# Kernel optimization log

Measured on AMD Instinct MI355X. Metric: run time of the kernel, lower is better.

## Reference

```python
import jax, jax.numpy as jnp
import numpy as np

B, LQ, LKV = 32, 512, 512
SIZE, H = 512, 8
HD = SIZE // H
SCALE = 1.0 / np.sqrt(HD)
LN_EPS = 1e-5


def layer_norm(x, w, b):
    mu = jnp.mean(x, axis=-1, keepdims=True)
    var = jnp.mean(jnp.square(x - mu), axis=-1, keepdims=True)
    return (x - mu) * jax.lax.rsqrt(var + LN_EPS) * w + b


def setup_inputs() -> dict:
    key = jax.random.key(0)
    ks = jax.random.split(key, 8)
    s = 0.02
    return {
        "query": jax.random.normal(ks[0], (B, LQ, SIZE), jnp.float32),
        "key_value": jax.random.normal(ks[1], (B, LKV, SIZE), jnp.float32),
        "Wq": jax.random.normal(ks[2], (SIZE, SIZE), jnp.float32) * s,
        "bq": jnp.zeros((SIZE,), jnp.float32),
        "Wk": jax.random.normal(ks[3], (SIZE, SIZE), jnp.float32) * s,
        "bk": jnp.zeros((SIZE,), jnp.float32),
        "Wv": jax.random.normal(ks[4], (SIZE, SIZE), jnp.float32) * s,
        "bv": jnp.zeros((SIZE,), jnp.float32),
        "Wo": jax.random.normal(ks[5], (SIZE, SIZE), jnp.float32) * s,
        "bo": jnp.zeros((SIZE,), jnp.float32),
        "ln0_w": jnp.ones((SIZE,), jnp.float32),
        "ln0_b": jnp.zeros((SIZE,), jnp.float32),
        "ln1_w": jnp.ones((SIZE,), jnp.float32),
        "ln1_b": jnp.zeros((SIZE,), jnp.float32),
    }


def reference(query, key_value, Wq, bq, Wk, bk, Wv, bv, Wo, bo, ln0_w, ln0_b, ln1_w, ln1_b):
    b, lq, _ = query.shape
    lkv = key_value.shape[1]
    # projections
    q = query @ Wq.T + bq          # [B, Lq, SIZE]
    k = key_value @ Wk.T + bk      # [B, Lkv, SIZE]
    v = key_value @ Wv.T + bv
    # split heads: torch cat(split(head_size, 2), 0) == [B,L,H,HD] view with head axis separate
    qh = q.reshape(b, lq, H, HD)
    kh = k.reshape(b, lkv, H, HD)
    vh = v.reshape(b, lkv, H, HD)
    # attention scores [B, H, Lq, Lkv]
    A_ = jnp.einsum("bqhd,bkhd->bhqk", qh, kh) * SCALE
    # signed softmax: tanh(A_) * softmax(sqrt(A_^2 + 0.01)) over keys
    A = jnp.tanh(A_) * jax.nn.softmax(jnp.sqrt(jnp.square(A_) + 0.01), axis=-1)
    # residual q + attention output, merge heads back
    oh = qh + jnp.einsum("bhqk,bkhd->bqhd", A, vh)   # [B, Lq, H, HD]
    output = oh.reshape(b, lq, SIZE)
    output = layer_norm(output, ln0_w, ln0_b)
    output = output + jax.nn.relu(output @ Wo.T + bo)
    output = layer_norm(output, ln1_w, ln1_b)
    return output
```

## Files before the change

kernel.cpp:

```cpp
#include <hip/hip_runtime.h>

#define SIZE_D 512
#define HEADS  8
#define HDIM   64
#define BATCH  32
#define SEQ    512
#define SCALE_F 0.125f
#define NROWS  (BATCH * SEQ)

typedef __attribute__((ext_vector_type(8))) short bf16x8;
typedef __attribute__((ext_vector_type(4))) float f32x4;
typedef __attribute__((ext_vector_type(4))) unsigned int u32x4;

__device__ __forceinline__ unsigned short f2bf(float f) {
    union { float f; unsigned int u; } c{f};
    unsigned int x = c.u;
    x += 0x7fffu + ((x >> 16) & 1u);
    return (unsigned short)(x >> 16);
}
__device__ __forceinline__ float bf2f(unsigned short u) {
    union { unsigned int i; float f; } c;
    c.i = (unsigned int)u << 16;
    return c.f;
}
__device__ __forceinline__ unsigned int pack2bf(float lo, float hi) {
    return ((__float_as_uint(hi) + 0x8000u) & 0xffff0000u) |
           ((__float_as_uint(lo) + 0x8000u) >> 16);
}
__device__ __forceinline__ void gload_lds16(const unsigned short* g, unsigned short* l) {
    __builtin_amdgcn_global_load_lds(
        (const __attribute__((address_space(1))) unsigned int*)g,
        (__attribute__((address_space(3))) unsigned int*)l, 16, 0, 0);
}

#define KBAR8() do {                                                      \
    asm volatile("s_waitcnt vmcnt(8) lgkmcnt(0)" ::: "memory");           \
    __builtin_amdgcn_sched_barrier(0);                                    \
    __builtin_amdgcn_s_barrier();                                         \
    __builtin_amdgcn_sched_barrier(0);                                    \
} while (0)
#define KBAR0() do {                                                      \
    asm volatile("s_waitcnt vmcnt(0) lgkmcnt(0)" ::: "memory");           \
    __builtin_amdgcn_sched_barrier(0);                                    \
    __builtin_amdgcn_s_barrier();                                         \
    __builtin_amdgcn_sched_barrier(0);                                    \
} while (0)

__global__ __launch_bounds__(256) void cvt_w4(const float* __restrict__ w0,
                                              const float* __restrict__ w1,
                                              const float* __restrict__ w2,
                                              const float* __restrict__ w3,
                                              unsigned short* __restrict__ d) {
    const float* srcs[4] = {w0, w1, w2, w3};
    const float* s = srcs[blockIdx.y];
    unsigned short* dst = d + (size_t)blockIdx.y * (SIZE_D * SIZE_D);
    const int n = SIZE_D * SIZE_D;
    const int stride = gridDim.x * blockDim.x * 4;
    for (int i = (blockIdx.x * blockDim.x + threadIdx.x) * 4; i < n; i += stride) {
        const float4 v = *reinterpret_cast<const float4*>(s + i);
        ushort4 o;
        o.x = f2bf(v.x); o.y = f2bf(v.y); o.z = f2bf(v.z); o.w = f2bf(v.w);
        *reinterpret_cast<ushort4*>(dst + i) = o;
    }
}

__global__ __launch_bounds__(256, 2) void gemm_proj3(const float* __restrict__ query,
                                                     const float* __restrict__ keyv,
                                                     const unsigned short* __restrict__ Wall,
                                                     const float* __restrict__ bq,
                                                     const float* __restrict__ bk,
                                                     const float* __restrict__ bv,
                                                     unsigned short* __restrict__ Qh,
                                                     unsigned short* __restrict__ Kh,
                                                     unsigned short* __restrict__ Vt) {
    __shared__ __align__(16) unsigned short Ad[2][128 * 64];
    __shared__ __align__(16) unsigned short Bd[2][128 * 64];

    const int tid  = threadIdx.x;
    const int wv   = tid >> 6;
    const int lane = tid & 63;
    const int y    = blockIdx.y;
    const int bm   = blockIdx.x * 128;
    const int bn   = y * 128;
    const int wr   = wv >> 1;
    const int wc   = wv & 1;

    const float* A = (y < 4) ? query : keyv;

    float4 areg[2][4][2];

    auto loadA = [&](int t, int slot) {
        const int k0 = t * 64;
#pragma unroll
        for (int i = 0; i < 4; ++i) {
            const int o   = (wv * 32 + i * 8) * 128 + lane * 16;
            const int row = o >> 7;
            const int col = ((o & 127) ^ ((row & 7) << 4)) >> 1;
            const float* src = A + (size_t)(bm + row) * SIZE_D + k0 + col;
            areg[slot][i][0] = *reinterpret_cast<const float4*>(src);
            areg[slot][i][1] = *reinterpret_cast<const float4*>(src + 4);
        }
    };
    auto writeA = [&](int buf, int slot) {
#pragma unroll
        for (int i = 0; i < 4; ++i) {
            const int o = (wv * 32 + i * 8) * 128 + lane * 16;
            union { unsigned int u[4]; bf16x8 v; } pk;
            pk.u[0] = pack2bf(areg[slot][i][0].x, areg[slot][i][0].y);
            pk.u[1] = pack2bf(areg[slot][i][0].z, areg[slot][i][0].w);
            pk.u[2] = pack2bf(areg[slot][i][1].x, areg[slot][i][1].y);
            pk.u[3] = pack2bf(areg[slot][i][1].z, areg[slot][i][1].w);
            *reinterpret_cast<bf16x8*>(&Ad[buf][o >> 1]) = pk.v;
        }
    };
    auto stageW = [&](int buf, int t) {
        const int k0 = t * 64;
#pragma unroll
        for (int i = 0; i < 4; ++i) {
            const int o   = (wv * 32 + i * 8) * 128 + lane * 16;
            const int row = o >> 7;
            const int col = ((o & 127) ^ ((row & 7) << 4)) >> 1;
            gload_lds16(Wall + (size_t)(bn + row) * SIZE_D + k0 + col, &Bd[buf][o >> 1]);
        }
    };

    f32x4 acc[4][4];
#pragma unroll
    for (int mt = 0; mt < 4; ++mt)
#pragma unroll
        for (int nt = 0; nt < 4; ++nt) acc[mt][nt] = (f32x4){0.f, 0.f, 0.f, 0.f};

    loadA(0, 0);
    stageW(0, 0);
    writeA(0, 0);
    loadA(1, 1);

#pragma unroll
    for (int t = 0; t < 8; ++t) {
        const int cur = t & 1;
        if (t < 7) { KBAR8(); } else { KBAR0(); }

        if (t < 7) stageW(cur ^ 1, t + 1);
        if (t < 6) loadA(t + 2, t & 1);

        bf16x8 af[2][4], bfr[2][4];
#pragma unroll
        for (int kc = 0; kc < 2; ++kc) {
#pragma unroll
            for (int mt = 0; mt < 4; ++mt) {
                const int r = wr * 64 + mt * 16 + (lane & 15);
                int byte = r * 128 + kc * 64 + (lane >> 4) * 16;
                byte ^= (r & 7) << 4;
                af[kc][mt] = *reinterpret_cast<const bf16x8*>(
                    reinterpret_cast<const char*>(&Ad[cur][0]) + byte);
            }
#pragma unroll
            for (int nt = 0; nt < 4; ++nt) {
                const int r = wc * 64 + nt * 16 + (lane & 15);
                int byte = r * 128 + kc * 64 + (lane >> 4) * 16;
                byte ^= (r & 7) << 4;
                bfr[kc][nt] = *reinterpret_cast<const bf16x8*>(
                    reinterpret_cast<const char*>(&Bd[cur][0]) + byte);
            }
        }
#pragma unroll
        for (int kc = 0; kc < 2; ++kc)
#pragma unroll
            for (int mt = 0; mt < 4; ++mt)
#pragma unroll
                for (int nt = 0; nt < 4; ++nt)
                    acc[mt][nt] = __builtin_amdgcn_mfma_f32_16x16x32_bf16(
                        af[kc][mt], bfr[kc][nt], acc[mt][nt], 0, 0, 0);

        if (t < 7) writeA(cur ^ 1, (t + 1) & 1);
    }

    if (y < 8) {
        const float* bias = (y < 4) ? bq : bk;
        unsigned short* D = (y < 4) ? Qh : Kh;
        const int coff = (y < 4) ? 0 : 512;
#pragma unroll
        for (int nt = 0; nt < 4; ++nt) {
            const int colL = bn - coff + wc * 64 + nt * 16 + (lane & 15);
            const float bc = bias[colL];
            const int h = colL >> 6, dd = colL & 63;
#pragma unroll
            for (int mt = 0; mt < 4; ++mt) {
                const int row0 = bm + wr * 64 + mt * 16 + (lane >> 4) * 4;
#pragma unroll
                for (int r = 0; r < 4; ++r) {
                    const int row = row0 + r;
                    const int b_ = row >> 9, l = row & 511;
                    float z = acc[mt][nt][r] + bc;
                    if (y >= 4) z *= SCALE_F;
                    D[(((size_t)b_ * HEADS + h) * SEQ + l) * HDIM + dd] = f2bf(z);
                }
            }
        }
    } else {
#pragma unroll
        for (int nt = 0; nt < 4; ++nt) {
            const int c2 = bn - 1024 + wc * 64 + nt * 16 + (lane & 15);
            const float bc = bv[c2];
            const int hV = c2 >> 6, dV = c2 & 63;
#pragma unroll
            for (int mt = 0; mt < 4; ++mt) {
                const int row0 = bm + wr * 64 + mt * 16 + (lane >> 4) * 4;
                const int b_ = row0 >> 9, kv = row0 & 511;
                ushort4 pk;
                pk.x = f2bf(acc[mt][nt][0] + bc);
                pk.y = f2bf(acc[mt][nt][1] + bc);
                pk.z = f2bf(acc[mt][nt][2] + bc);
                pk.w = f2bf(acc[mt][nt][3] + bc);
                *reinterpret_cast<ushort4*>(
                    &Vt[(((size_t)b_ * HEADS + hV) * HDIM + dV) * SEQ + kv]) = pk;
            }
        }
    }
}

__global__ __launch_bounds__(256, 2) void attn_mfma(const unsigned short* __restrict__ Qh,
                                                    const unsigned short* __restrict__ Kh,
                                                    const unsigned short* __restrict__ Vt,
                                                    unsigned short* __restrict__ outb) {
    __shared__ __align__(16) unsigned short Kt[2][64 * 64];
    __shared__ __align__(16) unsigned short Vs[2][64 * 64];

    const int tid  = threadIdx.x;
    const int wv   = tid >> 6;
    const int lane = tid & 63;
    const int bh   = blockIdx.x;
    const int b    = bh >> 3;
    const int h    = bh & 7;
    const int g    = lane >> 4;

    const unsigned short* Qb = Qh + (size_t)bh * (SEQ * HDIM);
    const unsigned short* Kb = Kh + (size_t)bh * (SEQ * HDIM);
    const unsigned short* Vb = Vt + (size_t)bh * (HDIM * SEQ);

    const int m0 = blockIdx.y * 256 + wv * 64;

    auto stageKV = [&](int buf, int t) {
        const int kv0 = t * 64;
#pragma unroll
        for (int i = 0; i < 2; ++i) {
            const int o   = i * 4096 + tid * 16;
            const int row = o >> 7;
            const int in  = (o & 127) ^ ((row & 7) << 4);
            gload_lds16(Kb + (size_t)(kv0 + row) * HDIM + (in >> 1), &Kt[buf][o >> 1]);
            gload_lds16(Vb + (size_t)row * SEQ + kv0 + (in >> 1), &Vs[buf][o >> 1]);
        }
    };

    bf16x8 qf[4][2];
#pragma unroll
    for (int mt = 0; mt < 4; ++mt)
#pragma unroll
        for (int kc = 0; kc < 2; ++kc) {
            const int m = m0 + mt * 16 + (lane & 15);
            union { u32x4 u; bf16x8 v; } cv;
            cv.u = *reinterpret_cast<const u32x4*>(
                Qb + (size_t)m * HDIM + kc * 32 + g * 8);
            qf[mt][kc] = cv.v;
        }

    f32x4 oacc[4][4];
    float esum[4] = {0.f, 0.f, 0.f, 0.f};
#pragma unroll
    for (int mt = 0; mt < 4; ++mt)
#pragma unroll
        for (int x = 0; x < 4; ++x) oacc[mt][x] = (f32x4){0.f, 0.f, 0.f, 0.f};

    stageKV(0, 0);
    __syncthreads();
    int cur = 0;

    for (int t = 0; t < 8; ++t) {
        if (t < 7) stageKV(cur ^ 1, t + 1);

        f32x4 sacc[4][4];
#pragma unroll
        for (int nt = 0; nt < 4; ++nt)
#pragma unroll
            for (int mt = 0; mt < 4; ++mt) sacc[nt][mt] = (f32x4){0.f, 0.f, 0.f, 0.f};

#pragma unroll
        for (int kc = 0; kc < 2; ++kc) {
            bf16x8 kf[4];
#pragma unroll
            for (int nt = 0; nt < 4; ++nt) {
                const int kvl = nt * 16 + (lane & 15);
                int byte = kvl * 128 + kc * 64 + g * 16;
                byte ^= (kvl & 7) << 4;
                kf[nt] = *reinterpret_cast<const bf16x8*>(
                    reinterpret_cast<const char*>(&Kt[cur][0]) + byte);
            }
            __builtin_amdgcn_s_setprio(1);
#pragma unroll
            for (int nt = 0; nt < 4; ++nt)
#pragma unroll
                for (int mt = 0; mt < 4; ++mt)
                    sacc[nt][mt] = __builtin_amdgcn_mfma_f32_16x16x32_bf16(
                        kf[nt], qf[mt][kc], sacc[nt][mt], 0, 0, 0);
            __builtin_amdgcn_s_setprio(0);
        }

        bf16x8 pa[2][4];
#pragma unroll
        for (int c = 0; c < 2; ++c)
#pragma unroll
            for (int mt = 0; mt < 4; ++mt) {
                float w[8];
#pragma unroll
                for (int j = 0; j < 8; ++j) {
                    const float s  = sacc[2 * c + (j >> 2)][mt][j & 3];
                    const float a  = fminf(fabsf(s), 30.0f);
                    const float tt = __expf(a);
                    const float t2 = tt * tt;
                    const float u  = __builtin_amdgcn_sqrtf(fmaf(s, s, 0.01f));
                    const float dl = u - a;
                    const float ed = fmaf(dl, fmaf(dl, 0.5f, 1.0f), 1.0f);
                    const float eu = tt * ed;
                    esum[mt] += eu;
                    const float th = fmaf(-2.0f, __builtin_amdgcn_rcpf(t2 + 1.0f), 1.0f);
                    w[j] = __builtin_copysignf(th * eu, s);
                }
                union { unsigned int u[4]; bf16x8 v; } pk;
#pragma unroll
                for (int p = 0; p < 4; ++p)
                    pk.u[p] = (__float_as_uint(w[2 * p + 1]) & 0xffff0000u) |
                              (__float_as_uint(w[2 * p]) >> 16);
                pa[c][mt] = pk.v;
            }

#pragma unroll
        for (int c = 0; c < 2; ++c) {
            bf16x8 vf[4];
#pragma unroll
            for (int dt = 0; dt < 4; ++dt) {
                const int d = dt * 16 + (lane & 15);
                const int swz = (d & 7) << 4;
                const int rowb = d * 128;
                uint2 lo = *reinterpret_cast<const uint2*>(
                    reinterpret_cast<const char*>(&Vs[cur][0]) +
                    (rowb + (((c * 32 + 4 * g) * 2) ^ swz)));
                uint2 hi = *reinterpret_cast<const uint2*>(
                    reinterpret_cast<const char*>(&Vs[cur][0]) +
                    (rowb + (((c * 32 + 16 + 4 * g) * 2) ^ swz)));
                union { unsigned int u[4]; bf16x8 v; } cvb;
                cvb.u[0] = lo.x; cvb.u[1] = lo.y;
                cvb.u[2] = hi.x; cvb.u[3] = hi.y;
                vf[dt] = cvb.v;
            }
            __builtin_amdgcn_s_setprio(1);
#pragma unroll
            for (int mt = 0; mt < 4; ++mt)
#pragma unroll
                for (int dt = 0; dt < 4; ++dt)
                    oacc[mt][dt] = __builtin_amdgcn_mfma_f32_16x16x32_bf16(
                        pa[c][mt], vf[dt], oacc[mt][dt], 0, 0, 0);
            __builtin_amdgcn_s_setprio(0);
        }

        __syncthreads();
        cur ^= 1;
    }

    float rden[4];
#pragma unroll
    for (int mt = 0; mt < 4; ++mt) {
        float e = esum[mt];
        e += __shfl_xor(e, 16);
        e += __shfl_xor(e, 32);
        rden[mt] = __builtin_amdgcn_rcpf(e);
    }
    float rr_[4][4];
#pragma unroll
    for (int mt = 0; mt < 4; ++mt)
#pragma unroll
        for (int r = 0; r < 4; ++r)
            rr_[mt][r] = __shfl(rden[mt], g * 4 + r);

#pragma unroll
    for (int mt = 0; mt < 4; ++mt)
#pragma unroll
        for (int dt = 0; dt < 4; ++dt)
#pragma unroll
            for (int r = 0; r < 4; ++r) {
                const int m = m0 + mt * 16 + g * 4 + r;
                const int d = dt * 16 + (lane & 15);
                const float qv = bf2f(Qb[(size_t)m * HDIM + d]);
                outb[((size_t)b * SEQ + m) * SIZE_D + h * HDIM + d] =
                    f2bf(qv + oacc[mt][dt][r] * rr_[mt][r]);
            }
}

__global__ __launch_bounds__(256) void ln0_bf16(const unsigned short* __restrict__ in,
                                                const float* __restrict__ w,
                                                const float* __restrict__ b,
                                                unsigned short* __restrict__ outb) {
    const int row = blockIdx.x;
    const int tid = threadIdx.x;
    const ushort2 xb = *reinterpret_cast<const ushort2*>(&in[(size_t)row * SIZE_D + tid * 2]);
    float2 x;
    x.x = bf2f(xb.x);
    x.y = bf2f(xb.y);

    float s  = x.x + x.y;
    float sq = x.x * x.x + x.y * x.y;
#pragma unroll
    for (int off = 32; off > 0; off >>= 1) {
        s  += __shfl_xor(s, off);
        sq += __shfl_xor(sq, off);
    }
    __shared__ float rs[4], rq[4];
    const int wv = tid >> 6;
    if ((tid & 63) == 0) { rs[wv] = s; rq[wv] = sq; }
    __syncthreads();
    s  = rs[0] + rs[1] + rs[2] + rs[3];
    sq = rq[0] + rq[1] + rq[2] + rq[3];

    const float mu  = s * (1.0f / SIZE_D);
    const float var = sq * (1.0f / SIZE_D) - mu * mu;
    const float rr  = rsqrtf(var + 1e-5f);

    const float2 wv2 = *reinterpret_cast<const float2*>(&w[tid * 2]);
    const float2 bv2 = *reinterpret_cast<const float2*>(&b[tid * 2]);
    ushort2 ob;
    ob.x = f2bf((x.x - mu) * rr * wv2.x + bv2.x);
    ob.y = f2bf((x.y - mu) * rr * wv2.y + bv2.y);
    *reinterpret_cast<ushort2*>(&outb[(size_t)row * SIZE_D + tid * 2]) = ob;
}

__global__ __launch_bounds__(512, 2) void oproj_ln(const unsigned short* __restrict__ X,
                                                   const unsigned short* __restrict__ W,
                                                   const float* __restrict__ bo,
                                                   const float* __restrict__ g1,
                                                   const float* __restrict__ b1,
                                                   float* __restrict__ out) {
    __shared__ __align__(16) unsigned short Ad[2][32 * 32];
    __shared__ __align__(16) unsigned short Bd[2][512 * 32];
    __shared__ float red[32][8][2];
    __shared__ float stat[32][2];

    const int tid  = threadIdx.x;
    const int wv   = tid >> 6;
    const int lane = tid & 63;
    const int bm   = blockIdx.x * 32;

    auto stage = [&](int buf, int t) {
        const int k0 = t * 32;
        if (tid < 128) {
            const int o   = tid * 16;
            const int row = o >> 6;
            const int in  = (o & 63) ^ (((row >> 1) & 3) << 4);
            gload_lds16(X + (size_t)(bm + row) * SIZE_D + k0 + (in >> 1), &Ad[buf][o >> 1]);
        }
#pragma unroll
        for (int i = 0; i < 4; ++i) {
            const int o   = i * 8192 + tid * 16;
            const int row = o >> 6;
            const int in  = (o & 63) ^ (((row >> 1) & 3) << 4);
            gload_lds16(W + (size_t)row * SIZE_D + k0 + (in >> 1), &Bd[buf][o >> 1]);
        }
    };

    f32x4 acc[2][4];
#pragma unroll
    for (int mt = 0; mt < 2; ++mt)
#pragma unroll
        for (int nt = 0; nt < 4; ++nt) acc[mt][nt] = (f32x4){0.f, 0.f, 0.f, 0.f};

    stage(0, 0);
    __syncthreads();
    int cur = 0;

    for (int t = 0; t < 16; ++t) {
        if (t < 15) stage(cur ^ 1, t + 1);

        bf16x8 af[2], bfr[4];
#pragma unroll
        for (int mt = 0; mt < 2; ++mt) {
            const int r = mt * 16 + (lane & 15);
            int byte = r * 64 + (lane >> 4) * 16;
            byte ^= ((r >> 1) & 3) << 4;
            af[mt] = *reinterpret_cast<const bf16x8*>(
                reinterpret_cast<const char*>(&Ad[cur][0]) + byte);
        }
#pragma unroll
        for (int nt = 0; nt < 4; ++nt) {
            const int r = wv * 64 + nt * 16 + (lane & 15);
            int byte = r * 64 + (lane >> 4) * 16;
            byte ^= ((r >> 1) & 3) << 4;
            bfr[nt] = *reinterpret_cast<const bf16x8*>(
                reinterpret_cast<const char*>(&Bd[cur][0]) + byte);
        }
#pragma unroll
        for (int mt = 0; mt < 2; ++mt)
#pragma unroll
            for (int nt = 0; nt < 4; ++nt)
                acc[mt][nt] = __builtin_amdgcn_mfma_f32_16x16x32_bf16(
                    af[mt], bfr[nt], acc[mt][nt], 0, 0, 0);

        __syncthreads();
        cur ^= 1;
    }

#pragma unroll
    for (int nt = 0; nt < 4; ++nt) {
        const int n  = wv * 64 + nt * 16 + (lane & 15);
        const float bc = bo[n];
#pragma unroll
        for (int mt = 0; mt < 2; ++mt) {
            const int row0 = bm + mt * 16 + (lane >> 4) * 4;
#pragma unroll
            for (int r = 0; r < 4; ++r) {
                const float R = bf2f(X[(size_t)(row0 + r) * SIZE_D + n]);
                acc[mt][nt][r] = R + fmaxf(acc[mt][nt][r] + bc, 0.0f);
            }
        }
    }

    float ps[2][4], pq[2][4];
#pragma unroll
    for (int mt = 0; mt < 2; ++mt)
#pragma unroll
        for (int r = 0; r < 4; ++r) {
            float s = 0.f, q = 0.f;
#pragma unroll
            for (int nt = 0; nt < 4; ++nt) {
                const float v = acc[mt][nt][r];
                s += v; q += v * v;
            }
#pragma unroll
            for (int off = 1; off <= 8; off <<= 1) {
                s += __shfl_xor(s, off);
                q += __shfl_xor(q, off);
            }
            ps[mt][r] = s; pq[mt][r] = q;
        }
    if ((lane & 15) < 8) {
        const int mtw = (lane & 15) >> 2;
        const int rw  = lane & 3;
        const int rowL = mtw * 16 + (lane >> 4) * 4 + rw;
        red[rowL][wv][0] = ps[mtw][rw];
        red[rowL][wv][1] = pq[mtw][rw];
    }
    __syncthreads();
    if (tid < 32) {
        float s = 0.f, q = 0.f;
#pragma unroll
        for (int w8 = 0; w8 < 8; ++w8) { s += red[tid][w8][0]; q += red[tid][w8][1]; }
        const float mu  = s * (1.0f / SIZE_D);
        const float var = q * (1.0f / SIZE_D) - mu * mu;
        stat[tid][0] = mu;
        stat[tid][1] = rsqrtf(var + 1e-5f);
    }
    __syncthreads();

#pragma unroll
    for (int nt = 0; nt < 4; ++nt) {
        const int n = wv * 64 + nt * 16 + (lane & 15);
        const float g = g1[n], bb = b1[n];
#pragma unroll
        for (int mt = 0; mt < 2; ++mt) {
#pragma unroll
            for (int r = 0; r < 4; ++r) {
                const int rowL = mt * 16 + (lane >> 4) * 4 + r;
                const float y = (acc[mt][nt][r] - stat[rowL][0]) * stat[rowL][1];
                out[(size_t)(bm + rowL) * SIZE_D + n] = y * g + bb;
            }
        }
    }
}

extern "C" void kernel_launch(void* const* d_in, const int* in_sizes, int n_in,
                              void* d_out, int out_size, void* d_ws, size_t ws_size,
                              hipStream_t stream) {
    const float* query = (const float*)d_in[0];
    const float* keyv  = (const float*)d_in[1];
    const float* Wq    = (const float*)d_in[2];
    const float* bq    = (const float*)d_in[3];
    const float* Wk    = (const float*)d_in[4];
    const float* bk    = (const float*)d_in[5];
    const float* Wv    = (const float*)d_in[6];
    const float* bv    = (const float*)d_in[7];
    const float* Wo    = (const float*)d_in[8];
    const float* bo    = (const float*)d_in[9];
    const float* ln0w  = (const float*)d_in[10];
    const float* ln0b  = (const float*)d_in[11];
    const float* ln1w  = (const float*)d_in[12];
    const float* ln1b  = (const float*)d_in[13];
    float* out = (float*)d_out;

    char* ws = (char*)d_ws;
    unsigned short* obf  = (unsigned short*)ws;
    unsigned short* Qh   = (unsigned short*)(ws + ((size_t)32 << 20));
    unsigned short* Xbf  = Qh;
    unsigned short* Kh   = (unsigned short*)(ws + ((size_t)48 << 20));
    unsigned short* Vt   = (unsigned short*)(ws + ((size_t)64 << 20));
    unsigned short* Wbf  = (unsigned short*)(ws + ((size_t)80 << 20));
    unsigned short* WoB  = Wbf + 786432;

    cvt_w4<<<dim3(64, 4), 256, 0, stream>>>(Wq, Wk, Wv, Wo, Wbf);

    gemm_proj3<<<dim3(128, 12), 256, 0, stream>>>(query, keyv, Wbf, bq, bk, bv, Qh, Kh, Vt);

    attn_mfma<<<dim3(BATCH * HEADS, 2), 256, 0, stream>>>(Qh, Kh, Vt, obf);

    ln0_bf16<<<NROWS, 256, 0, stream>>>(obf, ln0w, ln0b, Xbf);

    oproj_ln<<<NROWS / 32, 512, 0, stream>>>(Xbf, WoB, bo, ln1w, ln1b, out);
}
```

Baseline: 154.8 us.

## Quad-buffer attention KV tiles, halve barriers, and use one wave per row in LN0

The attention kernel now keeps four KV tile buffers in shared memory and stages two tiles ahead, processing two tiles per barrier, so there are half as many __syncthreads and loads have more time to overlap with compute. The clamp on |s| before exp is removed, which saves an instruction but could overflow if scores grow large. LayerNorm0 now gives each row to a single wavefront with 8-element vector loads, which removes the shared-memory reduction and block barrier and launches a quarter as many blocks. Doubling LDS per block to 64KB may reduce attention occupancy.

```diff
diff --git a/kernel.cpp b/kernel.cpp
--- a/kernel.cpp
+++ b/kernel.cpp
@@ -223,8 +223,8 @@
                                                     const unsigned short* __restrict__ Kh,
                                                     const unsigned short* __restrict__ Vt,
                                                     unsigned short* __restrict__ outb) {
-    __shared__ __align__(16) unsigned short Kt[2][64 * 64];
-    __shared__ __align__(16) unsigned short Vs[2][64 * 64];
+    __shared__ __align__(16) unsigned short Kt[4][64 * 64];
+    __shared__ __align__(16) unsigned short Vs[4][64 * 64];
 
     const int tid  = threadIdx.x;
     const int wv   = tid >> 6;
@@ -272,98 +272,105 @@
         for (int x = 0; x < 4; ++x) oacc[mt][x] = (f32x4){0.f, 0.f, 0.f, 0.f};
 
     stageKV(0, 0);
+    stageKV(1, 1);
     __syncthreads();
-    int cur = 0;
-
-    for (int t = 0; t < 8; ++t) {
-        if (t < 7) stageKV(cur ^ 1, t + 1);
-
-        f32x4 sacc[4][4];
-#pragma unroll
-        for (int nt = 0; nt < 4; ++nt)
-#pragma unroll
-            for (int mt = 0; mt < 4; ++mt) sacc[nt][mt] = (f32x4){0.f, 0.f, 0.f, 0.f};
-
-#pragma unroll
-        for (int kc = 0; kc < 2; ++kc) {
-            bf16x8 kf[4];
-#pragma unroll
-            for (int nt = 0; nt < 4; ++nt) {
-                const int kvl = nt * 16 + (lane & 15);
-                int byte = kvl * 128 + kc * 64 + g * 16;
-                byte ^= (kvl & 7) << 4;
-                kf[nt] = *reinterpret_cast<const bf16x8*>(
-                    reinterpret_cast<const char*>(&Kt[cur][0]) + byte);
-            }
-            __builtin_amdgcn_s_setprio(1);
+
+    for (int tt = 0; tt < 8; tt += 2) {
+        if (tt < 6) {
+            stageKV((tt + 2) & 3, tt + 2);
+            stageKV((tt + 3) & 3, tt + 3);
+        }
+
+#pragma unroll
+        for (int p = 0; p < 2; ++p) {
+            const int cur = (tt + p) & 3;
+
+            f32x4 sacc[4][4];
 #pragma unroll
             for (int nt = 0; nt < 4; ++nt)
 #pragma unroll
+                for (int mt = 0; mt < 4; ++mt) sacc[nt][mt] = (f32x4){0.f, 0.f, 0.f, 0.f};
+
+#pragma unroll
+            for (int kc = 0; kc < 2; ++kc) {
+                bf16x8 kf[4];
+#pragma unroll
+                for (int nt = 0; nt < 4; ++nt) {
+                    const int kvl = nt * 16 + (lane & 15);
+                    int byte = kvl * 128 + kc * 64 + g * 16;
+                    byte ^= (kvl & 7) << 4;
+                    kf[nt] = *reinterpret_cast<const bf16x8*>(
+                        reinterpret_cast<const char*>(&Kt[cur][0]) + byte);
+                }
+                __builtin_amdgcn_s_setprio(1);
+#pragma unroll
+                for (int nt = 0; nt < 4; ++nt)
+#pragma unroll
+                    for (int mt = 0; mt < 4; ++mt)
+                        sacc[nt][mt] = __builtin_amdgcn_mfma_f32_16x16x32_bf16(
+                            kf[nt], qf[mt][kc], sacc[nt][mt], 0, 0, 0);
+                __builtin_amdgcn_s_setprio(0);
+            }
+
+            bf16x8 pa[2][4];
+#pragma unroll
+            for (int c = 0; c < 2; ++c)
+#pragma unroll
+                for (int mt = 0; mt < 4; ++mt) {
+                    float w[8];
+#pragma unroll
+                    for (int j = 0; j < 8; ++j) {
+                        const float s  = sacc[2 * c + (j >> 2)][mt][j & 3];
+                        const float a  = fabsf(s);
+                        const float tt_ = __expf(a);
+                        const float t2 = tt_ * tt_;
+                        const float u  = __builtin_amdgcn_sqrtf(fmaf(s, s, 0.01f));
+                        const float dl = u - a;
+                        const float ed = fmaf(dl, fmaf(dl, 0.5f, 1.0f), 1.0f);
+                        const float eu = tt_ * ed;
+                        esum[mt] += eu;
+                        const float th = fmaf(-2.0f, __builtin_amdgcn_rcpf(t2 + 1.0f), 1.0f);
+                        w[j] = __builtin_copysignf(th * eu, s);
+                    }
+                    union { unsigned int u[4]; bf16x8 v; } pk;
+#pragma unroll
+                    for (int pp = 0; pp < 4; ++pp)
+                        pk.u[pp] = (__float_as_uint(w[2 * pp + 1]) & 0xffff0000u) |
+                                   (__float_as_uint(w[2 * pp]) >> 16);
+                    pa[c][mt] = pk.v;
+                }
+
+#pragma unroll
+            for (int c = 0; c < 2; ++c) {
+                bf16x8 vf[4];
+#pragma unroll
+                for (int dt = 0; dt < 4; ++dt) {
+                    const int d = dt * 16 + (lane & 15);
+                    const int swz = (d & 7) << 4;
+                    const int rowb = d * 128;
+                    uint2 lo = *reinterpret_cast<const uint2*>(
+                        reinterpret_cast<const char*>(&Vs[cur][0]) +
+                        (rowb + (((c * 32 + 4 * g) * 2) ^ swz)));
+                    uint2 hi = *reinterpret_cast<const uint2*>(
+                        reinterpret_cast<const char*>(&Vs[cur][0]) +
+                        (rowb + (((c * 32 + 16 + 4 * g) * 2) ^ swz)));
+                    union { unsigned int u[4]; bf16x8 v; } cvb;
+                    cvb.u[0] = lo.x; cvb.u[1] = lo.y;
+                    cvb.u[2] = hi.x; cvb.u[3] = hi.y;
+                    vf[dt] = cvb.v;
+                }
+                __builtin_amdgcn_s_setprio(1);
+#pragma unroll
                 for (int mt = 0; mt < 4; ++mt)
-                    sacc[nt][mt] = __builtin_amdgcn_mfma_f32_16x16x32_bf16(
-                        kf[nt], qf[mt][kc], sacc[nt][mt], 0, 0, 0);
-            __builtin_amdgcn_s_setprio(0);
-        }
-
-        bf16x8 pa[2][4];
-#pragma unroll
-        for (int c = 0; c < 2; ++c)
-#pragma unroll
-            for (int mt = 0; mt < 4; ++mt) {
-                float w[8];
-#pragma unroll
-                for (int j = 0; j < 8; ++j) {
-                    const float s  = sacc[2 * c + (j >> 2)][mt][j & 3];
-                    const float a  = fminf(fabsf(s), 30.0f);
-                    const float tt = __expf(a);
-                    const float t2 = tt * tt;
-                    const float u  = __builtin_amdgcn_sqrtf(fmaf(s, s, 0.01f));
-                    const float dl = u - a;
-                    const float ed = fmaf(dl, fmaf(dl, 0.5f, 1.0f), 1.0f);
-                    const float eu = tt * ed;
-                    esum[mt] += eu;
-                    const float th = fmaf(-2.0f, __builtin_amdgcn_rcpf(t2 + 1.0f), 1.0f);
-                    w[j] = __builtin_copysignf(th * eu, s);
-                }
-                union { unsigned int u[4]; bf16x8 v; } pk;
-#pragma unroll
-                for (int p = 0; p < 4; ++p)
-                    pk.u[p] = (__float_as_uint(w[2 * p + 1]) & 0xffff0000u) |
-                              (__float_as_uint(w[2 * p]) >> 16);
-                pa[c][mt] = pk.v;
-            }
-
-#pragma unroll
-        for (int c = 0; c < 2; ++c) {
-            bf16x8 vf[4];
-#pragma unroll
-            for (int dt = 0; dt < 4; ++dt) {
-                const int d = dt * 16 + (lane & 15);
-                const int swz = (d & 7) << 4;
-                const int rowb = d * 128;
-                uint2 lo = *reinterpret_cast<const uint2*>(
-                    reinterpret_cast<const char*>(&Vs[cur][0]) +
-                    (rowb + (((c * 32 + 4 * g) * 2) ^ swz)));
-                uint2 hi = *reinterpret_cast<const uint2*>(
-                    reinterpret_cast<const char*>(&Vs[cur][0]) +
-                    (rowb + (((c * 32 + 16 + 4 * g) * 2) ^ swz)));
-                union { unsigned int u[4]; bf16x8 v; } cvb;
-                cvb.u[0] = lo.x; cvb.u[1] = lo.y;
-                cvb.u[2] = hi.x; cvb.u[3] = hi.y;
-                vf[dt] = cvb.v;
-            }
-            __builtin_amdgcn_s_setprio(1);
-#pragma unroll
-            for (int mt = 0; mt < 4; ++mt)
-#pragma unroll
-                for (int dt = 0; dt < 4; ++dt)
-                    oacc[mt][dt] = __builtin_amdgcn_mfma_f32_16x16x32_bf16(
-                        pa[c][mt], vf[dt], oacc[mt][dt], 0, 0, 0);
-            __builtin_amdgcn_s_setprio(0);
+#pragma unroll
+                    for (int dt = 0; dt < 4; ++dt)
+                        oacc[mt][dt] = __builtin_amdgcn_mfma_f32_16x16x32_bf16(
+                            pa[c][mt], vf[dt], oacc[mt][dt], 0, 0, 0);
+                __builtin_amdgcn_s_setprio(0);
+            }
         }
 
         __syncthreads();
-        cur ^= 1;
     }
 
     float rden[4];
@@ -399,37 +406,42 @@
                                                 const float* __restrict__ w,
                                                 const float* __restrict__ b,
                                                 unsigned short* __restrict__ outb) {
-    const int row = blockIdx.x;
-    const int tid = threadIdx.x;
-    const ushort2 xb = *reinterpret_cast<const ushort2*>(&in[(size_t)row * SIZE_D + tid * 2]);
-    float2 x;
-    x.x = bf2f(xb.x);
-    x.y = bf2f(xb.y);
-
-    float s  = x.x + x.y;
-    float sq = x.x * x.x + x.y * x.y;
+    const int tid  = threadIdx.x;
+    const int lane = tid & 63;
+    const int row  = blockIdx.x * 4 + (tid >> 6);
+    const size_t base = (size_t)row * SIZE_D + lane * 8;
+
+    const ushort4 a0 = *reinterpret_cast<const ushort4*>(&in[base]);
+    const ushort4 a1 = *reinterpret_cast<const ushort4*>(&in[base + 4]);
+    float x[8];
+    x[0] = bf2f(a0.x); x[1] = bf2f(a0.y); x[2] = bf2f(a0.z); x[3] = bf2f(a0.w);
+    x[4] = bf2f(a1.x); x[5] = bf2f(a1.y); x[6] = bf2f(a1.z); x[7] = bf2f(a1.w);
+
+    float s = 0.f, sq = 0.f;
+#pragma unroll
+    for (int j = 0; j < 8; ++j) { s += x[j]; sq += x[j] * x[j]; }
 #pragma unroll
     for (int off = 32; off > 0; off >>= 1) {
         s  += __shfl_xor(s, off);
         sq += __shfl_xor(sq, off);
     }
-    __shared__ float rs[4], rq[4];
-    const int wv = tid >> 6;
-    if ((tid & 63) == 0) { rs[wv] = s; rq[wv] = sq; }
-    __syncthreads();
-    s  = rs[0] + rs[1] + rs[2] + rs[3];
-    sq = rq[0] + rq[1] + rq[2] + rq[3];
 
     const float mu  = s * (1.0f / SIZE_D);
     const float var = sq * (1.0f / SIZE_D) - mu * mu;
     const float rr  = rsqrtf(var + 1e-5f);
 
-    const float2 wv2 = *reinterpret_cast<const float2*>(&w[tid * 2]);
-    const float2 bv2 = *reinterpret_cast<const float2*>(&b[tid * 2]);
-    ushort2 ob;
-    ob.x = f2bf((x.x - mu) * rr * wv2.x + bv2.x);
-    ob.y = f2bf((x.y - mu) * rr * wv2.y + bv2.y);
-    *reinterpret_cast<ushort2*>(&outb[(size_t)row * SIZE_D + tid * 2]) = ob;
+    const float4 w0 = *reinterpret_cast<const float4*>(&w[lane * 8]);
+    const float4 w1 = *reinterpret_cast<const float4*>(&w[lane * 8 + 4]);
+    const float4 b0 = *reinterpret_cast<const float4*>(&b[lane * 8]);
+    const float4 b1 = *reinterpret_cast<const float4*>(&b[lane * 8 + 4]);
+    const float wa[8] = {w0.x, w0.y, w0.z, w0.w, w1.x, w1.y, w1.z, w1.w};
+    const float ba[8] = {b0.x, b0.y, b0.z, b0.w, b1.x, b1.y, b1.z, b1.w};
+
+    union { unsigned short s[8]; bf16x8 v; } o;
+#pragma unroll
+    for (int j = 0; j < 8; ++j)
+        o.s[j] = f2bf((x[j] - mu) * rr * wa[j] + ba[j]);
+    *reinterpret_cast<bf16x8*>(&outb[base]) = o.v;
 }
 
 __global__ __launch_bounds__(512, 2) void oproj_ln(const unsigned short* __restrict__ X,
@@ -608,7 +620,7 @@
 
     attn_mfma<<<dim3(BATCH * HEADS, 2), 256, 0, stream>>>(Qh, Kh, Vt, obf);
 
-    ln0_bf16<<<NROWS, 256, 0, stream>>>(obf, ln0w, ln0b, Xbf);
+    ln0_bf16<<<NROWS / 4, 256, 0, stream>>>(obf, ln0w, ln0b, Xbf);
 
     oproj_ln<<<NROWS / 32, 512, 0, stream>>>(Xbf, WoB, bo, ln1w, ln1b, out);
 }
```

Result: faster. 146.9 us, median of 2 (-5.1%).
